# Kernel optimization log

Measured on AMD Instinct MI355X. Metric: run time of the kernel, lower is better.

The kernel has to match this reference:

```python
import jax, jax.numpy as jnp
import numpy as np

N_NODES = 100000
N_EDGES = 1600000
IN_DIM, HID, OUT = 256, 128, 32


def setup_inputs() -> dict:
    key = jax.random.key(0)
    ks = jax.random.split(key, 8)
    x = jax.random.normal(ks[0], (N_NODES, IN_DIM), dtype=jnp.float32)
    edge_index = jax.random.randint(ks[1], (2, N_EDGES), 0, N_NODES, dtype=jnp.int64)
    # Glorot-ish small scale to keep activations stable
    W0 = jax.random.normal(ks[2], (IN_DIM, HID), dtype=jnp.float32) * 0.05
    W1 = jax.random.normal(ks[3], (HID, HID), dtype=jnp.float32) * 0.05
    W2 = jax.random.normal(ks[4], (HID, OUT), dtype=jnp.float32) * 0.05
    b0 = jnp.zeros((HID,), jnp.float32)
    b1 = jnp.zeros((HID,), jnp.float32)
    b2 = jnp.zeros((OUT,), jnp.float32)
    return {"x": x, "edge_index": edge_index, "W0": W0, "b0": b0,
            "W1": W1, "b1": b1, "W2": W2, "b2": b2}


def reference(x, edge_index, W0, b0, W1, b1, W2, b2):
    # PyG GCNConv: add self-loops, symmetric normalization D^-1/2 A D^-1/2,
    # messages flow src (row 0) -> dst (row 1), aggregated at dst.
    n = x.shape[0]
    src, dst = edge_index[0], edge_index[1]
    ones = jnp.ones((src.shape[0],), x.dtype)
    deg = jax.ops.segment_sum(ones, dst, num_segments=n) + 1.0  # +1 for self-loop
    dinv = jax.lax.rsqrt(deg)                                   # [N]
    edge_norm = dinv[src] * dinv[dst]                           # [E]
    self_norm = dinv * dinv                                     # [N] self-loop weight

    def gcn_conv(h, W, b):
        h = h @ W                                               # [N, D_out]
        agg = jax.ops.segment_sum(h[src] * edge_norm[:, None], dst, num_segments=n)
        return agg + h * self_norm[:, None] + b

    h = gcn_conv(x, W0, b0)
    # dropout after layers i != 0: identity in eval mode (deterministic reference)
    h = gcn_conv(h, W1, b1)
    h = gcn_conv(h, W2, b2)
    return jax.nn.log_softmax(h, axis=1)
```

## Files before the change

### kernel.cpp

```cpp
#include <hip/hip_runtime.h>
#include <hip/hip_bf16.h>
#include <type_traits>

#define N_NODES 100000
#define N_EDGES 1600000
#define SLICE_N 12500
#define CAP     64

typedef float f32x4 __attribute__((ext_vector_type(4)));
typedef _Float16 f16x8 __attribute__((ext_vector_type(8)));

__global__ __launch_bounds__(256) void fill_bucket_kernel(const int* __restrict__ esrc,
                                                          const int* __restrict__ edst,
                                                          int* __restrict__ cnt,
                                                          int* __restrict__ esorted) {
    const int slice = blockIdx.x & 7;
    const int chunk = blockIdx.x >> 3;
    const int base = chunk * 2048 + threadIdx.x;
    const int lo = slice * SLICE_N, hi = lo + SLICE_N;
    #pragma unroll
    for (int i = 0; i < 8; ++i) {
        int e = base + i * 256;
        if (e < N_EDGES) {
            int d = edst[e];
            if (d >= lo && d < hi) {
                int pos = atomicAdd(&cnt[d], 1);
                if (pos < CAP) esorted[(size_t)d * CAP + pos] = esrc[e];
            }
        }
    }
}

__global__ void dinv_kernel(const int* __restrict__ cnt, float* __restrict__ dinv) {
    int i = blockIdx.x * 256 + threadIdx.x;
    if (i < N_NODES) dinv[i] = 1.0f / sqrtf((float)cnt[i] + 1.0f);
}

__global__ void wconv_all_kernel(const float* __restrict__ W0, const float* __restrict__ W1,
                                 const float* __restrict__ W2, _Float16* __restrict__ Wt0,
                                 _Float16* __restrict__ Wt1, _Float16* __restrict__ Wt2) {
    int i = blockIdx.x * 256 + threadIdx.x;
    if (i < 32768) {
        int k = i / 128, col = i % 128;
        Wt0[col * 256 + k] = (_Float16)W0[i];
    } else if (i < 49152) {
        int j = i - 32768;
        int k = j / 128, col = j % 128;
        Wt1[col * 128 + k] = (_Float16)W1[j];
    } else if (i < 53248) {
        int j = i - 49152;
        int k = j / 32, col = j % 32;
        Wt2[col * 128 + k] = (_Float16)W2[j];
    }
}

#define LOADA(st, k0)                                                          \
    do {                                                                       \
        _Pragma("unroll")                                                      \
        for (int r = 0; r < 2; ++r) {                                          \
            const float* ap = A + (size_t)gr[r] * K + (k0) + kof;              \
            a32[st][r][0] = *(const f32x4*)ap;                                 \
            a32[st][r][1] = *(const f32x4*)(ap + 4);                           \
        }                                                                      \
    } while (0)

#define LOADB(st, k0)                                                          \
    do {                                                                       \
        _Pragma("unroll")                                                      \
        for (int c = 0; c < FC; ++c)                                           \
            bst[st][c] = *(const f16x8*)(Bt + (size_t)(c * 16 + l15) * K + (k0) + kof); \
    } while (0)

template<int K, int M>
__global__ __launch_bounds__(256) void mfma_gemm_f16(const float* __restrict__ A,
                                                     const _Float16* __restrict__ Bt,
                                                     const float* __restrict__ dinv,
                                                     _Float16* __restrict__ C) {
    constexpr int FC = M / 16;
    constexpr int NIT = K / 32;
    const int tid = threadIdx.x;
    const int wave = tid >> 6, lane = tid & 63;
    const int row0 = blockIdx.x * 128;
    const int r0 = wave * 32;
    const int l15 = lane & 15, kof = (lane >> 4) * 8;

    f32x4 acc[2][FC] = {};
    int gr[2];
    #pragma unroll
    for (int r = 0; r < 2; ++r) {
        int g = row0 + r0 + r * 16 + l15;
        gr[r] = (g < N_NODES) ? g : N_NODES - 1;
    }

    f32x4 a32[3][2][2];
    f16x8 bst[2][FC];

    LOADA(0, 0);
    if (NIT > 1) LOADA(1, 32);
    LOADB(0, 0);

    #pragma unroll
    for (int it = 0; it < NIT; ++it) {
        if (it + 2 < NIT) LOADA((it + 2) % 3, (it + 2) * 32);
        if (it + 1 < NIT) LOADB((it + 1) % 2, (it + 1) * 32);
        f16x8 af[2];
        #pragma unroll
        for (int r = 0; r < 2; ++r) {
            #pragma unroll
            for (int j = 0; j < 4; ++j) {
                af[r][j] = (_Float16)a32[it % 3][r][0][j];
                af[r][4 + j] = (_Float16)a32[it % 3][r][1][j];
            }
        }
        #pragma unroll
        for (int c = 0; c < FC; ++c)
            #pragma unroll
            for (int r = 0; r < 2; ++r)
                acc[r][c] = __builtin_amdgcn_mfma_f32_16x16x32_f16(af[r], bst[it % 2][c], acc[r][c], 0, 0, 0);
    }

    #pragma unroll
    for (int r = 0; r < 2; ++r) {
        #pragma unroll
        for (int j = 0; j < 4; ++j) {
            int g = row0 + r0 + r * 16 + (lane >> 4) * 4 + j;
            if (g >= N_NODES) continue;
            float s = dinv[g];
            #pragma unroll
            for (int c = 0; c < FC; ++c)
                C[(size_t)g * M + c * 16 + l15] = (_Float16)(acc[r][c][j] * s);
        }
    }
}

template<int OUTC>
__global__ __launch_bounds__(256) void gather_gemm_kernel(const int* __restrict__ cnt,
                                                          const int* __restrict__ esorted,
                                                          const float* __restrict__ dinv,
                                                          const f16x8* __restrict__ hs,
                                                          const float* __restrict__ bias,
                                                          const _Float16* __restrict__ Wt,
                                                          _Float16* __restrict__ outh) {
    __shared__ _Float16 Ws[OUTC][136];
    __shared__ _Float16 As[16][136];
    const int tid = threadIdx.x;

    #pragma unroll
    for (int i = tid; i < OUTC * 16; i += 256) {
        int col = i >> 4, c8 = i & 15;
        *(f16x8*)&Ws[col][c8 * 8] = *(const f16x8*)(Wt + (size_t)col * 128 + c8 * 8);
    }

    const int n16 = tid >> 4;
    const int lane = tid & 15;
    const int node = blockIdx.x * 16 + n16;
    {
        int len = cnt[node]; if (len > CAP) len = CAP;
        const int* __restrict__ lst = esorted + (size_t)node * CAP;
        float dn = dinv[node];
        f16x8 hv = hs[(size_t)node * 16 + lane];
        float acc[8];
        #pragma unroll
        for (int d = 0; d < 8; ++d) acc[d] = (float)hv[d];
        int j = 0;
        for (; j + 8 <= len; j += 8) {
            int s[8];
            f16x8 v[8];
            #pragma unroll
            for (int k = 0; k < 8; ++k) s[k] = lst[j + k];
            #pragma unroll
            for (int k = 0; k < 8; ++k) v[k] = hs[(size_t)s[k] * 16 + lane];
            #pragma unroll
            for (int k = 0; k < 8; ++k)
                #pragma unroll
                for (int d = 0; d < 8; ++d) acc[d] += (float)v[k][d];
        }
        for (; j < len; ++j) {
            f16x8 v = hs[(size_t)lst[j] * 16 + lane];
            #pragma unroll
            for (int d = 0; d < 8; ++d) acc[d] += (float)v[d];
        }
        const float* bp = bias + lane * 8;
        f16x8 o;
        #pragma unroll
        for (int d = 0; d < 8; ++d) o[d] = (_Float16)(acc[d] * dn + bp[d]);
        *(f16x8*)&As[n16][lane * 8] = o;
    }
    __syncthreads();

    const int wave = tid >> 6, l64 = tid & 63;
    const int l15 = l64 & 15, kq = l64 >> 4;
    constexpr int NF = OUTC / 16;
    constexpr int FPW = (NF + 3) / 4;
    #pragma unroll
    for (int f = 0; f < FPW; ++f) {
        int cf = wave * FPW + f;
        if (cf < NF) {
            int col = cf * 16 + l15;
            f32x4 a2 = {};
            #pragma unroll
            for (int it = 0; it < 4; ++it) {
                f16x8 af = *(const f16x8*)&As[l15][it * 32 + kq * 8];
                f16x8 bf = *(const f16x8*)&Ws[col][it * 32 + kq * 8];
                a2 = __builtin_amdgcn_mfma_f32_16x16x32_f16(af, bf, a2, 0, 0, 0);
            }
            #pragma unroll
            for (int j = 0; j < 4; ++j) {
                int g = blockIdx.x * 16 + kq * 4 + j;
                outh[(size_t)g * OUTC + col] = (_Float16)(a2[j] * dinv[g]);
            }
        }
    }
}

__global__ __launch_bounds__(256) void gather_lsm_kernel(const int* __restrict__ cnt,
                                                         const int* __restrict__ esorted,
                                                         const float* __restrict__ dinv,
                                                         const f16x8* __restrict__ hs,
                                                         const float* __restrict__ bias,
                                                         float* __restrict__ out) {
    constexpr int R = 4;
    int gid = blockIdx.x * blockDim.x + threadIdx.x;
    int node = gid / 4;
    int lane = gid % 4;
    if (node >= N_NODES) return;
    int len = cnt[node]; if (len > CAP) len = CAP;
    const int* __restrict__ lst = esorted + (size_t)node * CAP;
    float dn = dinv[node];
    f16x8 hv = hs[(size_t)node * R + lane];
    float acc[8];
    #pragma unroll
    for (int d = 0; d < 8; ++d) acc[d] = (float)hv[d];
    int j = 0;
    for (; j + 8 <= len; j += 8) {
        int s[8];
        f16x8 v[8];
        #pragma unroll
        for (int k = 0; k < 8; ++k) s[k] = lst[j + k];
        #pragma unroll
        for (int k = 0; k < 8; ++k) v[k] = hs[(size_t)s[k] * R + lane];
        #pragma unroll
        for (int k = 0; k < 8; ++k)
            #pragma unroll
            for (int d = 0; d < 8; ++d) acc[d] += (float)v[k][d];
    }
    for (; j < len; ++j) {
        f16x8 v = hs[(size_t)lst[j] * R + lane];
        #pragma unroll
        for (int d = 0; d < 8; ++d) acc[d] += (float)v[d];
    }
    const float* bp = bias + lane * 8;
    float o[8];
    #pragma unroll
    for (int d = 0; d < 8; ++d) o[d] = acc[d] * dn + bp[d];
    float m = o[0];
    #pragma unroll
    for (int d = 1; d < 8; ++d) m = fmaxf(m, o[d]);
    m = fmaxf(m, __shfl_xor(m, 1, 4));
    m = fmaxf(m, __shfl_xor(m, 2, 4));
    float s = 0.f;
    #pragma unroll
    for (int d = 0; d < 8; ++d) s += expf(o[d] - m);
    s += __shfl_xor(s, 1, 4);
    s += __shfl_xor(s, 2, 4);
    float ls = m + logf(s);
    f32x4 r0, r1;
    #pragma unroll
    for (int d = 0; d < 4; ++d) { r0[d] = o[d] - ls; r1[d] = o[4 + d] - ls; }
    f32x4* op = (f32x4*)out + (size_t)node * 8 + lane * 2;
    op[0] = r0;
    op[1] = r1;
}

extern "C" void kernel_launch(void* const* d_in, const int* in_sizes, int n_in,
                              void* d_out, int out_size, void* d_ws, size_t ws_size,
                              hipStream_t stream) {
    const float* x  = (const float*)d_in[0];
    const int*   ei = (const int*)d_in[1];
    const float* W0 = (const float*)d_in[2];
    const float* b0 = (const float*)d_in[3];
    const float* W1 = (const float*)d_in[4];
    const float* b1 = (const float*)d_in[5];
    const float* W2 = (const float*)d_in[6];
    const float* b2 = (const float*)d_in[7];
    float* out = (float*)d_out;

    char* ws = (char*)d_ws;
    float* dinv    = (float*)(ws + 0);
    int*   cnt     = (int*)  (ws + (512 << 10));
    int*   esorted = (int*)  (ws + (1 << 20));
    _Float16* Wt0  = (_Float16*)(ws + 27262976);
    _Float16* Wt1  = (_Float16*)(ws + 27262976 + 65536);
    _Float16* Wt2  = (_Float16*)(ws + 27262976 + 98304);
    _Float16* hs   = (_Float16*)(ws + 28311552);
    _Float16* hs1  = (_Float16*)(ws + 28311552 + 26214400);
    _Float16* hs2  = (_Float16*)(ws + 28311552 + 52428800);
    const int* esrc = ei;
    const int* edst = ei + N_EDGES;

    const int NB = (N_NODES + 255) / 256;

    (void)hipMemsetAsync(cnt, 0, N_NODES * sizeof(int), stream);
    wconv_all_kernel<<<208, 256, 0, stream>>>(W0, W1, W2, Wt0, Wt1, Wt2);
    {
        const int chunks = (N_EDGES + 2047) / 2048;
        fill_bucket_kernel<<<chunks * 8, 256, 0, stream>>>(esrc, edst, cnt, esorted);
    }
    dinv_kernel<<<NB, 256, 0, stream>>>(cnt, dinv);

    const int RB128 = (N_NODES + 127) / 128;

    mfma_gemm_f16<256, 128><<<RB128, 256, 0, stream>>>(x, Wt0, dinv, hs);

    gather_gemm_kernel<128><<<N_NODES / 16, 256, 0, stream>>>(
        cnt, esorted, dinv, (const f16x8*)hs, b0, Wt1, hs1);

    gather_gemm_kernel<32><<<N_NODES / 16, 256, 0, stream>>>(
        cnt, esorted, dinv, (const f16x8*)hs1, b1, Wt2, hs2);

    gather_lsm_kernel<<<(N_NODES * 4 + 255) / 256, 256, 0, stream>>>(
        cnt, esorted, dinv, (const f16x8*)hs2, b2, out);
}
```

Measured before the change: 316.6 us.

## Fuse edge bucketing with first GEMM and move degree scaling into gathers

Merges the edge-bucket fill kernel and the first MFMA GEMM into one launch that interleaves one GEMM tile block with eight fill blocks. The goal is to overlap the atomic-heavy bucketing with the compute-heavy GEMM. Because dinv is not ready when that GEMM runs, the source-side normalization moves out of the GEMM epilogues and into the gather loops, which now load dinv[src] per edge and use FMAs. The gather-GEMM kernels also stop staging W in shared memory and read it straight from global memory. In exchange, every aggregation does extra random dinv loads.

```diff
diff --git a/kernel.cpp b/kernel.cpp
--- a/kernel.cpp
+++ b/kernel.cpp
@@ -9,32 +9,6 @@
 
 typedef float f32x4 __attribute__((ext_vector_type(4)));
 typedef _Float16 f16x8 __attribute__((ext_vector_type(8)));
-
-__global__ __launch_bounds__(256) void fill_bucket_kernel(const int* __restrict__ esrc,
-                                                          const int* __restrict__ edst,
-                                                          int* __restrict__ cnt,
-                                                          int* __restrict__ esorted) {
-    const int slice = blockIdx.x & 7;
-    const int chunk = blockIdx.x >> 3;
-    const int base = chunk * 2048 + threadIdx.x;
-    const int lo = slice * SLICE_N, hi = lo + SLICE_N;
-    #pragma unroll
-    for (int i = 0; i < 8; ++i) {
-        int e = base + i * 256;
-        if (e < N_EDGES) {
-            int d = edst[e];
-            if (d >= lo && d < hi) {
-                int pos = atomicAdd(&cnt[d], 1);
-                if (pos < CAP) esorted[(size_t)d * CAP + pos] = esrc[e];
-            }
-        }
-    }
-}
-
-__global__ void dinv_kernel(const int* __restrict__ cnt, float* __restrict__ dinv) {
-    int i = blockIdx.x * 256 + threadIdx.x;
-    if (i < N_NODES) dinv[i] = 1.0f / sqrtf((float)cnt[i] + 1.0f);
-}
 
 __global__ void wconv_all_kernel(const float* __restrict__ W0, const float* __restrict__ W1,
                                  const float* __restrict__ W2, _Float16* __restrict__ Wt0,
@@ -54,6 +28,11 @@
     }
 }
 
+__global__ void dinv_kernel(const int* __restrict__ cnt, float* __restrict__ dinv) {
+    int i = blockIdx.x * 256 + threadIdx.x;
+    if (i < N_NODES) dinv[i] = 1.0f / sqrtf((float)cnt[i] + 1.0f);
+}
+
 #define LOADA(st, k0)                                                          \
     do {                                                                       \
         _Pragma("unroll")                                                      \
@@ -72,15 +51,14 @@
     } while (0)
 
 template<int K, int M>
-__global__ __launch_bounds__(256) void mfma_gemm_f16(const float* __restrict__ A,
-                                                     const _Float16* __restrict__ Bt,
-                                                     const float* __restrict__ dinv,
-                                                     _Float16* __restrict__ C) {
+__device__ __forceinline__ void gemm_tile_body(const float* __restrict__ A,
+                                               const _Float16* __restrict__ Bt,
+                                               _Float16* __restrict__ C,
+                                               int blk, int tid) {
     constexpr int FC = M / 16;
     constexpr int NIT = K / 32;
-    const int tid = threadIdx.x;
     const int wave = tid >> 6, lane = tid & 63;
-    const int row0 = blockIdx.x * 128;
+    const int row0 = blk * 128;
     const int r0 = wave * 32;
     const int l15 = lane & 15, kof = (lane >> 4) * 8;
 
@@ -125,10 +103,40 @@
         for (int j = 0; j < 4; ++j) {
             int g = row0 + r0 + r * 16 + (lane >> 4) * 4 + j;
             if (g >= N_NODES) continue;
-            float s = dinv[g];
             #pragma unroll
             for (int c = 0; c < FC; ++c)
-                C[(size_t)g * M + c * 16 + l15] = (_Float16)(acc[r][c][j] * s);
+                C[(size_t)g * M + c * 16 + l15] = (_Float16)acc[r][c][j];
+        }
+    }
+}
+
+__global__ __launch_bounds__(256) void fused_fill_gemm0(const int* __restrict__ esrc,
+                                                        const int* __restrict__ edst,
+                                                        int* __restrict__ cnt,
+                                                        int* __restrict__ esorted,
+                                                        const float* __restrict__ x,
+                                                        const _Float16* __restrict__ Wt0,
+                                                        _Float16* __restrict__ h) {
+    const int b = blockIdx.x;
+    const int g = b / 9;
+    if (b % 9 == 0) {
+        gemm_tile_body<256, 128>(x, Wt0, h, g, threadIdx.x);
+        return;
+    }
+    const int f = b - g - 1;
+    const int slice = b & 7;
+    const int chunk = f >> 3;
+    const int base = chunk * 2048 + threadIdx.x;
+    const int lo = slice * SLICE_N, hi = lo + SLICE_N;
+    #pragma unroll
+    for (int i = 0; i < 8; ++i) {
+        int e = base + i * 256;
+        if (e < N_EDGES) {
+            int d = edst[e];
+            if (d >= lo && d < hi) {
+                int pos = atomicAdd(&cnt[d], 1);
+                if (pos < CAP) esorted[(size_t)d * CAP + pos] = esrc[e];
+            }
         }
     }
 }
@@ -141,16 +149,8 @@
                                                           const float* __restrict__ bias,
                                                           const _Float16* __restrict__ Wt,
                                                           _Float16* __restrict__ outh) {
-    __shared__ _Float16 Ws[OUTC][136];
     __shared__ _Float16 As[16][136];
     const int tid = threadIdx.x;
-
-    #pragma unroll
-    for (int i = tid; i < OUTC * 16; i += 256) {
-        int col = i >> 4, c8 = i & 15;
-        *(f16x8*)&Ws[col][c8 * 8] = *(const f16x8*)(Wt + (size_t)col * 128 + c8 * 8);
-    }
-
     const int n16 = tid >> 4;
     const int lane = tid & 15;
     const int node = blockIdx.x * 16 + n16;
@@ -161,24 +161,27 @@
         f16x8 hv = hs[(size_t)node * 16 + lane];
         float acc[8];
         #pragma unroll
-        for (int d = 0; d < 8; ++d) acc[d] = (float)hv[d];
+        for (int d = 0; d < 8; ++d) acc[d] = dn * (float)hv[d];
         int j = 0;
         for (; j + 8 <= len; j += 8) {
             int s[8];
+            float ds_[8];
             f16x8 v[8];
             #pragma unroll
             for (int k = 0; k < 8; ++k) s[k] = lst[j + k];
             #pragma unroll
-            for (int k = 0; k < 8; ++k) v[k] = hs[(size_t)s[k] * 16 + lane];
+            for (int k = 0; k < 8; ++k) { ds_[k] = dinv[s[k]]; v[k] = hs[(size_t)s[k] * 16 + lane]; }
             #pragma unroll
             for (int k = 0; k < 8; ++k)
                 #pragma unroll
-                for (int d = 0; d < 8; ++d) acc[d] += (float)v[k][d];
+                for (int d = 0; d < 8; ++d) acc[d] = fmaf(ds_[k], (float)v[k][d], acc[d]);
         }
         for (; j < len; ++j) {
-            f16x8 v = hs[(size_t)lst[j] * 16 + lane];
-            #pragma unroll
-            for (int d = 0; d < 8; ++d) acc[d] += (float)v[d];
+            int s = lst[j];
+            float ds_ = dinv[s];
+            f16x8 v = hs[(size_t)s * 16 + lane];
+            #pragma unroll
+            for (int d = 0; d < 8; ++d) acc[d] = fmaf(ds_, (float)v[d], acc[d]);
         }
         const float* bp = bias + lane * 8;
         f16x8 o;
@@ -201,13 +204,13 @@
             #pragma unroll
             for (int it = 0; it < 4; ++it) {
                 f16x8 af = *(const f16x8*)&As[l15][it * 32 + kq * 8];
-                f16x8 bf = *(const f16x8*)&Ws[col][it * 32 + kq * 8];
+                f16x8 bf = *(const f16x8*)(Wt + (size_t)col * 128 + it * 32 + kq * 8);
                 a2 = __builtin_amdgcn_mfma_f32_16x16x32_f16(af, bf, a2, 0, 0, 0);
             }
             #pragma unroll
             for (int j = 0; j < 4; ++j) {
                 int g = blockIdx.x * 16 + kq * 4 + j;
-                outh[(size_t)g * OUTC + col] = (_Float16)(a2[j] * dinv[g]);
+                outh[(size_t)g * OUTC + col] = (_Float16)a2[j];
             }
         }
     }
@@ -230,24 +233,27 @@
     f16x8 hv = hs[(size_t)node * R + lane];
     float acc[8];
     #pragma unroll
-    for (int d = 0; d < 8; ++d) acc[d] = (float)hv[d];
+    for (int d = 0; d < 8; ++d) acc[d] = dn * (float)hv[d];
     int j = 0;
     for (; j + 8 <= len; j += 8) {
         int s[8];
+        float ds_[8];
         f16x8 v[8];
         #pragma unroll
         for (int k = 0; k < 8; ++k) s[k] = lst[j + k];
         #pragma unroll
-        for (int k = 0; k < 8; ++k) v[k] = hs[(size_t)s[k] * R + lane];
+        for (int k = 0; k < 8; ++k) { ds_[k] = dinv[s[k]]; v[k] = hs[(size_t)s[k] * R + lane]; }
         #pragma unroll
         for (int k = 0; k < 8; ++k)
             #pragma unroll
-            for (int d = 0; d < 8; ++d) acc[d] += (float)v[k][d];
+            for (int d = 0; d < 8; ++d) acc[d] = fmaf(ds_[k], (float)v[k][d], acc[d]);
     }
     for (; j < len; ++j) {
-        f16x8 v = hs[(size_t)lst[j] * R + lane];
-        #pragma unroll
-        for (int d = 0; d < 8; ++d) acc[d] += (float)v[d];
+        int s = lst[j];
+        float ds_ = dinv[s];
+        f16x8 v = hs[(size_t)s * R + lane];
+        #pragma unroll
+        for (int d = 0; d < 8; ++d) acc[d] = fmaf(ds_, (float)v[d], acc[d]);
     }
     const float* bp = bias + lane * 8;
     float o[8];
@@ -292,9 +298,9 @@
     _Float16* Wt0  = (_Float16*)(ws + 27262976);
     _Float16* Wt1  = (_Float16*)(ws + 27262976 + 65536);
     _Float16* Wt2  = (_Float16*)(ws + 27262976 + 98304);
-    _Float16* hs   = (_Float16*)(ws + 28311552);
-    _Float16* hs1  = (_Float16*)(ws + 28311552 + 26214400);
-    _Float16* hs2  = (_Float16*)(ws + 28311552 + 52428800);
+    _Float16* h0   = (_Float16*)(ws + 28311552);
+    _Float16* h1   = (_Float16*)(ws + 28311552 + 26214400);
+    _Float16* h2   = (_Float16*)(ws + 28311552 + 52428800);
     const int* esrc = ei;
     const int* edst = ei + N_EDGES;
 
@@ -302,22 +308,15 @@
 
     (void)hipMemsetAsync(cnt, 0, N_NODES * sizeof(int), stream);
     wconv_all_kernel<<<208, 256, 0, stream>>>(W0, W1, W2, Wt0, Wt1, Wt2);
-    {
-        const int chunks = (N_EDGES + 2047) / 2048;
-        fill_bucket_kernel<<<chunks * 8, 256, 0, stream>>>(esrc, edst, cnt, esorted);
-    }
+    fused_fill_gemm0<<<782 * 9, 256, 0, stream>>>(esrc, edst, cnt, esorted, x, Wt0, h0);
     dinv_kernel<<<NB, 256, 0, stream>>>(cnt, dinv);
 
-    const int RB128 = (N_NODES + 127) / 128;
-
-    mfma_gemm_f16<256, 128><<<RB128, 256, 0, stream>>>(x, Wt0, dinv, hs);
-
     gather_gemm_kernel<128><<<N_NODES / 16, 256, 0, stream>>>(
-        cnt, esorted, dinv, (const f16x8*)hs, b0, Wt1, hs1);
+        cnt, esorted, dinv, (const f16x8*)h0, b0, Wt1, h1);
 
     gather_gemm_kernel<32><<<N_NODES / 16, 256, 0, stream>>>(
-        cnt, esorted, dinv, (const f16x8*)hs1, b1, Wt2, hs2);
+        cnt, esorted, dinv, (const f16x8*)h1, b1, Wt2, h2);
 
     gather_lsm_kernel<<<(N_NODES * 4 + 255) / 256, 256, 0, stream>>>(
-        cnt, esorted, dinv, (const f16x8*)hs2, b2, out);
-}
+        cnt, esorted, dinv, (const f16x8*)h2, b2, out);
+}
```

After: 320.2 us. About the same (+1.2%).
